# Kernel optimization log

Hardware: AMD Instinct MI355X
Metric: run time of the kernel (lower is better)

Reference implementation:

```python
import jax, jax.numpy as jnp
import numpy as np

DIM = 768
HEADS = 12
FRAMES = 16
T = FRAMES // 2          # temporal length per stream = 8
N = 196                  # spatial patch tokens (14x14)
B = 16                   # batch
SCALE = (DIM // HEADS) ** -0.5


def setup_inputs() -> dict:
    key = jax.random.key(0)
    ks = jax.random.split(key, 10)
    return {
        "s_x": jax.random.normal(ks[0], (N + 1, B * T, DIM), jnp.float32),
        "t_x": jax.random.normal(ks[1], (B, T * N, DIM), jnp.float32),
        "clip_time_pos": SCALE * jax.random.normal(ks[2], (T, DIM), jnp.float32),
        "vmae_time_pos": SCALE * jax.random.normal(ks[3], (T, DIM), jnp.float32),
        "Wq": jax.random.normal(ks[4], (DIM, DIM), jnp.float32) * 0.02,
        "q_bias": jnp.zeros((DIM,), jnp.float32),
        "Wkv": jax.random.normal(ks[5], (2 * DIM, DIM), jnp.float32) * 0.02,
        "kv_bias": jnp.zeros((2 * DIM,), jnp.float32),
        "Wproj": jax.random.normal(ks[6], (DIM, DIM), jnp.float32) * 0.02,
        "proj_bias": jnp.zeros((DIM,), jnp.float32),
    }


def reference(s_x, t_x, clip_time_pos, vmae_time_pos,
              Wq, q_bias, Wkv, kv_bias, Wproj, proj_bias):
    b = t_x.shape[0]
    t = s_x.shape[1] // b            # = FRAMES // 2
    n = s_x.shape[0] - 1             # spatial tokens (CLS excluded)
    d = s_x.shape[-1]
    h = HEADS
    hd = d // h
    scale = hd ** -0.5

    s_cls = s_x[0]                                   # [b*t, d]
    # 'n (b t) d -> (b n) t d'
    s_pat = s_x[1:].reshape(n, b, t, d).transpose(1, 0, 2, 3).reshape(b * n, t, d)
    s_pat = s_pat + clip_time_pos                    # [(b n), t, d]
    # 'b (t n) d -> (b n) t d'
    tx = t_x.reshape(b, t, n, d).transpose(0, 2, 1, 3).reshape(b * n, t, d)
    tx = tx + vmae_time_pos

    # projections (bias added manually as in F.linear with explicit bias)
    q = (s_pat @ Wq.T + q_bias).reshape(b * n, t, h, hd).transpose(0, 2, 1, 3)  # [bn,h,t,hd]
    kv = (tx @ Wkv.T + kv_bias).reshape(b * n, t, 2, h, hd)                      # e outermost in (e h d)
    k = kv[:, :, 0].transpose(0, 2, 1, 3)            # [bn,h,t,hd]
    v = kv[:, :, 1].transpose(0, 2, 1, 3)

    attn = jax.nn.softmax(jnp.einsum('bhqd,bhkd->bhqk', q * scale, k), axis=-1)
    out = jnp.einsum('bhqk,bhkd->bhqd', attn, v)     # [bn,h,t,hd]
    out = out.transpose(0, 2, 1, 3).reshape(b * n, t, d)
    out = out @ Wproj.T + proj_bias
    # '(b n) t d -> n (b t) d'
    out = out.reshape(b, n, t, d).transpose(1, 0, 2, 3).reshape(n, b * t, d)
    return jnp.concatenate([s_cls[None], out], axis=0)
```

## Files before the change

### kernel.cpp

```cpp
#include <hip/hip_runtime.h>
#include <stdint.h>

#define DIM   768
#define NTOK  196
#define TT    8
#define MROWS 25088
#define HEADS 12
#define NKT   12

typedef __bf16 bf16x8 __attribute__((ext_vector_type(8)));
typedef float  f32x4  __attribute__((ext_vector_type(4)));
typedef unsigned short u16x4 __attribute__((ext_vector_type(4)));
typedef unsigned short u16x8 __attribute__((ext_vector_type(8)));

typedef __attribute__((address_space(1))) const void GAS;
typedef __attribute__((address_space(3))) void LAS;

__device__ inline unsigned short f2bf(float f) {
  uint32_t u = __builtin_bit_cast(uint32_t, f);
  u += 0x7FFFu + ((u >> 16) & 1u);
  return (unsigned short)(u >> 16);
}
__device__ inline float bf2f(unsigned short s) {
  uint32_t u = ((uint32_t)s) << 16;
  return __builtin_bit_cast(float, u);
}
__device__ inline void gl_lds16(const unsigned short* g, unsigned short* l) {
  __builtin_amdgcn_global_load_lds((GAS*)g, (LAS*)l, 16, 0, 0);
}
__device__ inline int xcd_swz(int orig, int nwg) {
  int xcd = orig & 7, loc = orig >> 3;
  int q = nwg >> 3, r = nwg & 7;
  int base = (xcd < r) ? xcd * (q + 1) : r * (q + 1) + (xcd - r) * q;
  return base + loc;
}

#define WAITV(n) asm volatile("s_waitcnt vmcnt(" #n ")" ::: "memory")

__global__ void wprep_kernel(const float* __restrict__ wq,
                             const float* __restrict__ wkv,
                             const float* __restrict__ wproj,
                             unsigned short* __restrict__ out) {
  int idx4 = blockIdx.x * blockDim.x + threadIdx.x;
  const int total4 = 2359296 / 4;
  if (idx4 >= total4) return;
  int e = idx4 * 4;
  const float* src; int off;
  if (e < 589824)        { src = wq;    off = e; }
  else if (e < 1769472)  { src = wkv;   off = e - 589824; }
  else                   { src = wproj; off = e - 1769472; }
  f32x4 v = *reinterpret_cast<const f32x4*>(&src[off]);
  u16x4 o;
  o[0] = f2bf(v[0]); o[1] = f2bf(v[1]); o[2] = f2bf(v[2]); o[3] = f2bf(v[3]);
  *reinterpret_cast<u16x4*>(&out[e]) = o;
}

__global__ void cls_kernel(const float* __restrict__ sx, float* __restrict__ out) {
  int i4 = blockIdx.x * blockDim.x + threadIdx.x;
  if (i4 < (128 * 768) / 4)
    reinterpret_cast<f32x4*>(out)[i4] = reinterpret_cast<const f32x4*>(sx)[i4];
}

template<int MODE>
__global__ __launch_bounds__(256)
void aprep_kernel(const float* __restrict__ src, const float* __restrict__ timepos,
                  unsigned short* __restrict__ dst) {
  int idx = blockIdx.x * blockDim.x + threadIdx.x;
  const int total = MROWS * (DIM / 8);
  if (idx >= total) return;
  int m  = idx / 96;
  int c8 = (idx - m * 96) * 8;
  int bn = m >> 3, t = m & 7;
  int b  = bn / NTOK, n = bn - b * NTOK;
  int srow = (MODE == 0) ? ((1 + n) * 128 + b * 8 + t)
                         : (b * (TT * NTOK) + t * NTOK + n);
  const float* sp = &src[srow * DIM + c8];
  const float* pp = &timepos[t * DIM + c8];
  f32x4 a0 = reinterpret_cast<const f32x4*>(sp)[0];
  f32x4 a1 = reinterpret_cast<const f32x4*>(sp)[1];
  f32x4 p0 = reinterpret_cast<const f32x4*>(pp)[0];
  f32x4 p1 = reinterpret_cast<const f32x4*>(pp)[1];
  a0 += p0; a1 += p1;
  u16x8 o;
  o[0] = f2bf(a0[0]); o[1] = f2bf(a0[1]); o[2] = f2bf(a0[2]); o[3] = f2bf(a0[3]);
  o[4] = f2bf(a1[0]); o[5] = f2bf(a1[1]); o[6] = f2bf(a1[2]); o[7] = f2bf(a1[3]);
  *reinterpret_cast<u16x8*>(&dst[m * DIM + c8]) = o;
}

template<int MODE>
__global__ __launch_bounds__(512)
void gemm8(const unsigned short* __restrict__ As,
           const unsigned short* __restrict__ At,
           const unsigned short* __restrict__ W0,
           const unsigned short* __restrict__ W1,
           const float* __restrict__ b0,
           const float* __restrict__ b1,
           unsigned short* __restrict__ out0,
           unsigned short* __restrict__ out1,
           float* __restrict__ fout,
           int bid0) {
  __shared__ unsigned short SB[3 * 24576];

  const int tid  = threadIdx.x;
  const int lane = tid & 63;
  const int w    = tid >> 6;
  const int wm   = w >> 2;
  const int wn   = w & 3;

  int bid = xcd_swz(blockIdx.x, gridDim.x) + bid0;

  const unsigned short *Ag, *Wg;
  const float* bias;
  unsigned short* ob = nullptr;
  int rt, ct, Ncols;
  float scale = 1.0f;
  if (MODE == 0) {
    if (bid < 588) { rt = bid / 6;  ct = bid % 6;  Ag = As; Wg = W0; bias = b0; ob = out0; Ncols = 768;  scale = 0.125f; }
    else { int b2 = bid - 588; rt = b2 / 12; ct = b2 % 12; Ag = At; Wg = W1; bias = b1; ob = out1; Ncols = 1536; }
  } else {
    rt = bid / 6; ct = bid % 6; Ag = As; Wg = W0; bias = b0; Ncols = 768;
  }
  const int m0 = rt * 256;
  const int n0 = ct * 128;

  auto stageA = [&](int kt) {
    const int kb = kt * 64;
    unsigned short* dst = &SB[(kt % 3) * 24576];
    #pragma unroll
    for (int rnd = 0; rnd < 4; ++rnd) {
      int s    = rnd * 8 + w;
      int srow = s * 8 + (lane >> 3);
      int scol = ((lane & 7) * 8) ^ ((srow & 7) << 3);
      gl_lds16(&Ag[(size_t)(m0 + srow) * 768 + kb + scol], dst + s * 512);
    }
  };
  auto stageB = [&](int kt) {
    const int kb = kt * 64;
    unsigned short* dst = &SB[(kt % 3) * 24576 + 16384];
    #pragma unroll
    for (int rnd = 0; rnd < 2; ++rnd) {
      int s    = rnd * 8 + w;
      int srow = s * 8 + (lane >> 3);
      int scol = ((lane & 7) * 8) ^ ((srow & 7) << 3);
      gl_lds16(&Wg[(size_t)(n0 + srow) * 768 + kb + scol], dst + s * 512);
    }
  };

  f32x4 acc[8][2] = {};

  stageA(0); stageB(0);
  stageA(1); stageB(1);

  for (int kt = 0; kt < NKT; ++kt) {
    __builtin_amdgcn_sched_barrier(0);
    if (kt < NKT - 1) { WAITV(6); } else { WAITV(0); }
    __builtin_amdgcn_s_barrier();
    asm volatile("" ::: "memory");

    const unsigned short* Ab = &SB[(kt % 3) * 24576];
    const unsigned short* Bb = Ab + 16384;
    const bool st = (kt + 2) < NKT;

    if (st) stageA(kt + 2);
    __builtin_amdgcn_sched_barrier(0);

    #pragma unroll
    for (int ks = 0; ks < 2; ++ks) {
      bf16x8 af[8], bfv[2];
      const int kc = ks * 32 + (lane >> 4) * 8;
      #pragma unroll
      for (int fm = 0; fm < 8; ++fm) {
        int r = wm * 128 + fm * 16 + (lane & 15);
        af[fm] = *reinterpret_cast<const bf16x8*>(&Ab[r * 64 + (kc ^ ((r & 7) << 3))]);
      }
      #pragma unroll
      for (int fn = 0; fn < 2; ++fn) {
        int r = wn * 32 + fn * 16 + (lane & 15);
        bfv[fn] = *reinterpret_cast<const bf16x8*>(&Bb[r * 64 + (kc ^ ((r & 7) << 3))]);
      }
      __builtin_amdgcn_s_setprio(1);
      #pragma unroll
      for (int fm = 0; fm < 8; ++fm)
        #pragma unroll
        for (int fn = 0; fn < 2; ++fn)
          acc[fm][fn] = __builtin_amdgcn_mfma_f32_16x16x32_bf16(af[fm], bfv[fn], acc[fm][fn], 0, 0, 0);
      __builtin_amdgcn_s_setprio(0);
      if (ks == 0 && st) stageB(kt + 2);
      __builtin_amdgcn_sched_barrier(0);
    }
  }

  #pragma unroll
  for (int fm = 0; fm < 8; ++fm) {
    #pragma unroll
    for (int fn = 0; fn < 2; ++fn) {
      int col = n0 + wn * 32 + fn * 16 + (lane & 15);
      float bsv = bias[col];
      #pragma unroll
      for (int i = 0; i < 4; ++i) {
        int row = m0 + wm * 128 + fm * 16 + (lane >> 4) * 4 + i;
        float v = acc[fm][fn][i] + bsv;
        if (MODE == 0) {
          v *= scale;
          ob[(size_t)row * Ncols + col] = f2bf(v);
        } else {
          int bn = row >> 3, t = row & 7;
          int b  = bn / NTOK, n = bn - b * NTOK;
          fout[((1 + n) * 128 + b * 8 + t) * DIM + col] = v;
        }
      }
    }
  }
}

__global__ __launch_bounds__(256)
void attn_kernel(const unsigned short* __restrict__ qb,
                 const unsigned short* __restrict__ kvb,
                 unsigned short* __restrict__ ob) {
  __shared__ __align__(16) float lds[4][3][8][68];
  const int tid  = threadIdx.x;
  const int lane = tid & 63;
  const int w    = tid >> 6;
  const int wid  = blockIdx.x * 4 + w;
  const int bn   = wid / HEADS;
  const int h    = wid - bn * HEADS;

  const int t  = lane >> 3;
  const int d0 = (lane & 7) * 8;
  const int qoff = (bn * 8 + t) * DIM + h * 64 + d0;
  const int koff = (bn * 8 + t) * (2 * DIM) + h * 64 + d0;

  u16x8 q8 = *reinterpret_cast<const u16x8*>(&qb[qoff]);
  u16x8 k8 = *reinterpret_cast<const u16x8*>(&kvb[koff]);
  u16x8 v8 = *reinterpret_cast<const u16x8*>(&kvb[koff + DIM]);
  f32x4 qa, qc, ka, kc, va, vc;
  #pragma unroll
  for (int e = 0; e < 4; ++e) {
    qa[e] = bf2f(q8[e]); qc[e] = bf2f(q8[e + 4]);
    ka[e] = bf2f(k8[e]); kc[e] = bf2f(k8[e + 4]);
    va[e] = bf2f(v8[e]); vc[e] = bf2f(v8[e + 4]);
  }
  *reinterpret_cast<f32x4*>(&lds[w][0][t][d0])     = qa;
  *reinterpret_cast<f32x4*>(&lds[w][0][t][d0 + 4]) = qc;
  *reinterpret_cast<f32x4*>(&lds[w][1][t][d0])     = ka;
  *reinterpret_cast<f32x4*>(&lds[w][1][t][d0 + 4]) = kc;
  *reinterpret_cast<f32x4*>(&lds[w][2][t][d0])     = va;
  *reinterpret_cast<f32x4*>(&lds[w][2][t][d0 + 4]) = vc;
  __syncthreads();

  const int i = lane >> 3, j = lane & 7;
  const f32x4* qi = reinterpret_cast<const f32x4*>(&lds[w][0][i][0]);
  const f32x4* kj = reinterpret_cast<const f32x4*>(&lds[w][1][j][0]);
  float s = 0.f;
  #pragma unroll
  for (int c = 0; c < 16; ++c) {
    f32x4 a = qi[c], b = kj[c];
    s += a[0] * b[0] + a[1] * b[1] + a[2] * b[2] + a[3] * b[3];
  }
  float m = s;
  m = fmaxf(m, __shfl_xor(m, 1));
  m = fmaxf(m, __shfl_xor(m, 2));
  m = fmaxf(m, __shfl_xor(m, 4));
  float e = __expf(s - m);
  float sum = e;
  sum += __shfl_xor(sum, 1);
  sum += __shfl_xor(sum, 2);
  sum += __shfl_xor(sum, 4);
  float p = e / sum;

  float o[8] = {};
  #pragma unroll
  for (int jj = 0; jj < 8; ++jj) {
    float pj = __shfl(p, (lane & 56) | jj);
    const f32x4* vj = reinterpret_cast<const f32x4*>(&lds[w][2][jj][d0]);
    f32x4 v0 = vj[0], v1 = vj[1];
    o[0] += pj * v0[0]; o[1] += pj * v0[1]; o[2] += pj * v0[2]; o[3] += pj * v0[3];
    o[4] += pj * v1[0]; o[5] += pj * v1[1]; o[6] += pj * v1[2]; o[7] += pj * v1[3];
  }
  u16x8 os;
  #pragma unroll
  for (int e2 = 0; e2 < 8; ++e2) os[e2] = f2bf(o[e2]);
  *reinterpret_cast<u16x8*>(&ob[qoff]) = os;
}

extern "C" void kernel_launch(void* const* d_in, const int* in_sizes, int n_in,
                              void* d_out, int out_size, void* d_ws, size_t ws_size,
                              hipStream_t stream) {
  const float* s_x       = (const float*)d_in[0];
  const float* t_x       = (const float*)d_in[1];
  const float* clip_pos  = (const float*)d_in[2];
  const float* vmae_pos  = (const float*)d_in[3];
  const float* Wq        = (const float*)d_in[4];
  const float* q_bias    = (const float*)d_in[5];
  const float* Wkv       = (const float*)d_in[6];
  const float* kv_bias   = (const float*)d_in[7];
  const float* Wproj     = (const float*)d_in[8];
  const float* proj_bias = (const float*)d_in[9];
  float* out = (float*)d_out;

  char* ws = (char*)d_ws;
  unsigned short* w_bf = (unsigned short*)ws;
  const size_t ABUF = 38535168, KVB = 77070336, WB = 4718592;
  const bool merged = ws_size >= (WB + 3 * ABUF + KVB);

  const unsigned short* wq_bf = w_bf;
  const unsigned short* wkv_bf = w_bf + 589824;
  const unsigned short* wpj_bf = w_bf + 1769472;

  const int prep_blocks = (MROWS * 96 + 255) / 256;

  wprep_kernel<<<dim3((589824 + 255) / 256), dim3(256), 0, stream>>>(Wq, Wkv, Wproj, w_bf);
  cls_kernel<<<dim3(96), dim3(256), 0, stream>>>(s_x, out);

  if (merged) {
    unsigned short* As    = (unsigned short*)(ws + WB);
    unsigned short* At    = (unsigned short*)(ws + WB + ABUF);
    unsigned short* q_bf  = (unsigned short*)(ws + WB + 2 * ABUF);
    unsigned short* kv_bf = (unsigned short*)(ws + WB + 3 * ABUF);
    aprep_kernel<0><<<dim3(prep_blocks), dim3(256), 0, stream>>>(s_x, clip_pos, As);
    aprep_kernel<1><<<dim3(prep_blocks), dim3(256), 0, stream>>>(t_x, vmae_pos, At);
    gemm8<0><<<dim3(1764), dim3(512), 0, stream>>>(As, At, wq_bf, wkv_bf, q_bias, kv_bias,
                                                   q_bf, kv_bf, nullptr, 0);
    attn_kernel<<<dim3(9408), dim3(256), 0, stream>>>(q_bf, kv_bf, As);
    gemm8<1><<<dim3(588), dim3(512), 0, stream>>>(As, nullptr, wpj_bf, nullptr, proj_bias,
                                                  nullptr, nullptr, nullptr, out, 0);
  } else {
    unsigned short* buf1  = (unsigned short*)(ws + WB);
    unsigned short* q_bf  = (unsigned short*)(ws + WB + ABUF);
    unsigned short* kv_bf = (unsigned short*)(ws + WB + 2 * ABUF);
    aprep_kernel<0><<<dim3(prep_blocks), dim3(256), 0, stream>>>(s_x, clip_pos, buf1);
    gemm8<0><<<dim3(588), dim3(512), 0, stream>>>(buf1, buf1, wq_bf, wkv_bf, q_bias, kv_bias,
                                                  q_bf, kv_bf, nullptr, 0);
    aprep_kernel<1><<<dim3(prep_blocks), dim3(256), 0, stream>>>(t_x, vmae_pos, buf1);
    gemm8<0><<<dim3(1176), dim3(512), 0, stream>>>(buf1, buf1, wq_bf, wkv_bf, q_bias, kv_bias,
                                                   q_bf, kv_bf, nullptr, 588);
    attn_kernel<<<dim3(9408), dim3(256), 0, stream>>>(q_bf, kv_bf, buf1);
    gemm8<1><<<dim3(588), dim3(512), 0, stream>>>(buf1, nullptr, wpj_bf, nullptr, proj_bias,
                                                  nullptr, nullptr, nullptr, out, 0);
  }
}
```

Measured before the change: 212.4 us.

## Use 256x256 ping-pong tiled GEMM with quadrant phases for Q/KV projections

Measured after the change: 220.7 us. 3.9% more time.

```diff
diff --git a/kernel.cpp b/kernel.cpp
--- a/kernel.cpp
+++ b/kernel.cpp
@@ -36,6 +36,8 @@
 }
 
 #define WAITV(n) asm volatile("s_waitcnt vmcnt(" #n ")" ::: "memory")
+#define CFENCE   asm volatile("" ::: "memory")
+#define TBAR     do { CFENCE; __builtin_amdgcn_s_barrier(); CFENCE; } while (0)
 
 __global__ void wprep_kernel(const float* __restrict__ wq,
                              const float* __restrict__ wkv,
@@ -87,20 +89,58 @@
   *reinterpret_cast<u16x8*>(&dst[m * DIM + c8]) = o;
 }
 
-template<int MODE>
-__global__ __launch_bounds__(512)
-void gemm8(const unsigned short* __restrict__ As,
-           const unsigned short* __restrict__ At,
-           const unsigned short* __restrict__ W0,
-           const unsigned short* __restrict__ W1,
-           const float* __restrict__ b0,
-           const float* __restrict__ b1,
-           unsigned short* __restrict__ out0,
-           unsigned short* __restrict__ out1,
-           float* __restrict__ fout,
-           int bid0) {
-  __shared__ unsigned short SB[3 * 24576];
-
+#define PHASE(buf, mq, nq, RA, STG)                                           \
+  {                                                                           \
+    const unsigned short* As_ = &SB[((buf) * 4 + (mq)) * 8192];               \
+    const unsigned short* Bs_ = &SB[((buf) * 4 + 2 + (nq)) * 8192];           \
+    if (RA) {                                                                 \
+      _Pragma("unroll")                                                       \
+      for (int ks = 0; ks < 2; ++ks)                                          \
+        _Pragma("unroll")                                                     \
+        for (int fm = 0; fm < 4; ++fm) {                                      \
+          int r = wm * 64 + fm * 16 + (lane & 15);                            \
+          int c = ks * 32 + (lane >> 4) * 8;                                  \
+          af[ks][fm] = *reinterpret_cast<const bf16x8*>(                      \
+              &As_[r * 64 + (c ^ ((r & 7) << 3))]);                           \
+        }                                                                     \
+    }                                                                         \
+    bf16x8 bfv[2][2];                                                         \
+    _Pragma("unroll")                                                         \
+    for (int ks = 0; ks < 2; ++ks)                                            \
+      _Pragma("unroll")                                                       \
+      for (int fn = 0; fn < 2; ++fn) {                                        \
+        int r = wn * 32 + fn * 16 + (lane & 15);                              \
+        int c = ks * 32 + (lane >> 4) * 8;                                    \
+        bfv[ks][fn] = *reinterpret_cast<const bf16x8*>(                       \
+            &Bs_[r * 64 + (c ^ ((r & 7) << 3))]);                             \
+      }                                                                       \
+    STG;                                                                      \
+    TBAR;                                                                     \
+    asm volatile("s_waitcnt lgkmcnt(0)" ::: "memory");                        \
+    __builtin_amdgcn_sched_barrier(0);                                        \
+    __builtin_amdgcn_s_setprio(1);                                            \
+    _Pragma("unroll")                                                         \
+    for (int ks = 0; ks < 2; ++ks)                                            \
+      _Pragma("unroll")                                                       \
+      for (int fm = 0; fm < 4; ++fm)                                          \
+        _Pragma("unroll")                                                     \
+        for (int fn = 0; fn < 2; ++fn)                                        \
+          acc[mq][nq][fm][fn] = __builtin_amdgcn_mfma_f32_16x16x32_bf16(      \
+              af[ks][fm], bfv[ks][fn], acc[mq][nq][fm][fn], 0, 0, 0);         \
+    __builtin_amdgcn_s_setprio(0);                                            \
+  }
+
+__global__ __launch_bounds__(512, 1)
+void gemm8p(const unsigned short* __restrict__ As,
+            const unsigned short* __restrict__ At,
+            const unsigned short* __restrict__ Wqb,
+            const unsigned short* __restrict__ Wkvb,
+            const float* __restrict__ bq,
+            const float* __restrict__ bkv,
+            unsigned short* __restrict__ qo,
+            unsigned short* __restrict__ kvo,
+            int bid0) {
+  __shared__ unsigned short SB[8 * 8192];
   const int tid  = threadIdx.x;
   const int lane = tid & 63;
   const int w    = tid >> 6;
@@ -108,20 +148,100 @@
   const int wn   = w & 3;
 
   int bid = xcd_swz(blockIdx.x, gridDim.x) + bid0;
-
-  const unsigned short *Ag, *Wg;
-  const float* bias;
-  unsigned short* ob = nullptr;
-  int rt, ct, Ncols;
-  float scale = 1.0f;
-  if (MODE == 0) {
-    if (bid < 588) { rt = bid / 6;  ct = bid % 6;  Ag = As; Wg = W0; bias = b0; ob = out0; Ncols = 768;  scale = 0.125f; }
-    else { int b2 = bid - 588; rt = b2 / 12; ct = b2 % 12; Ag = At; Wg = W1; bias = b1; ob = out1; Ncols = 1536; }
-  } else {
-    rt = bid / 6; ct = bid % 6; Ag = As; Wg = W0; bias = b0; Ncols = 768;
-  }
-  const int m0 = rt * 256;
-  const int n0 = ct * 128;
+  const unsigned short *Ag, *Wg; const float* bias;
+  unsigned short* ob; int rt, ct, Ncols; bool isq;
+  if (bid < 294) { isq = true;  rt = bid / 3; ct = bid % 3; Ag = As; Wg = Wqb;  bias = bq;  ob = qo;  Ncols = 768; }
+  else { isq = false; int b2 = bid - 294; rt = b2 / 6; ct = b2 % 6; Ag = At; Wg = Wkvb; bias = bkv; ob = kvo; Ncols = 1536; }
+  const int m0 = rt * 256, n0 = ct * 256;
+
+  float bsv[2][2];
+  #pragma unroll
+  for (int q = 0; q < 2; ++q)
+    #pragma unroll
+    for (int fn = 0; fn < 2; ++fn)
+      bsv[q][fn] = bias[n0 + q * 128 + wn * 32 + fn * 16 + (lane & 15)];
+
+  auto stage = [&](int slot, const unsigned short* src, int base_row, int kt) {
+    unsigned short* dst = &SB[slot * 8192];
+    #pragma unroll
+    for (int rr = 0; rr < 2; ++rr) {
+      int srow = rr * 64 + w * 8 + (lane >> 3);
+      int scol = ((lane & 7) * 8) ^ ((srow & 7) << 3);
+      gl_lds16(&src[(size_t)(base_row + srow) * DIM + kt * 64 + scol],
+               dst + (rr * 512 + w * 64) * 8);
+    }
+  };
+
+  f32x4 acc[2][2][4][2] = {};
+
+  stage(0, Ag, m0,       0);
+  stage(1, Ag, m0 + 128, 0);
+  stage(2, Wg, n0,       0);
+  stage(3, Wg, n0 + 128, 0);
+  stage(4, Ag, m0,       1);
+  stage(6, Wg, n0,       1);
+  WAITV(4);
+  TBAR;
+
+  for (int i = 0; i < NKT / 2; ++i) {
+    const int kt1 = 2 * i + 1, kt2 = 2 * i + 2, kt3 = 2 * i + 3;
+    const bool g2 = kt2 < NKT, g3 = kt3 < NKT, last = (i == NKT / 2 - 1);
+    bf16x8 af[2][4];
+
+    PHASE(0, 0, 0, 1, (stage(5, Ag, m0 + 128, kt1)));
+    TBAR;
+    PHASE(0, 0, 1, 0, (stage(7, Wg, n0 + 128, kt1)));
+    TBAR;
+    PHASE(0, 1, 0, 1, (g2 ? stage(0, Ag, m0, kt2) : void()));
+    TBAR;
+    PHASE(0, 1, 1, 0, (g2 ? stage(2, Wg, n0, kt2) : void()));
+    if (last) { WAITV(0); } else { WAITV(4); }
+    TBAR;
+    PHASE(1, 0, 0, 1, (g2 ? stage(1, Ag, m0 + 128, kt2) : void()));
+    TBAR;
+    PHASE(1, 0, 1, 0, (g2 ? stage(3, Wg, n0 + 128, kt2) : void()));
+    TBAR;
+    PHASE(1, 1, 0, 1, (g3 ? stage(4, Ag, m0, kt3) : void()));
+    TBAR;
+    PHASE(1, 1, 1, 0, (g3 ? stage(6, Wg, n0, kt3) : void()));
+    if (!last) { WAITV(4); }
+    TBAR;
+  }
+
+  #pragma unroll
+  for (int mq = 0; mq < 2; ++mq)
+    #pragma unroll
+    for (int nq = 0; nq < 2; ++nq)
+      #pragma unroll
+      for (int fm = 0; fm < 4; ++fm)
+        #pragma unroll
+        for (int fn = 0; fn < 2; ++fn) {
+          int col = n0 + nq * 128 + wn * 32 + fn * 16 + (lane & 15);
+          #pragma unroll
+          for (int ii = 0; ii < 4; ++ii) {
+            int row = m0 + mq * 128 + wm * 64 + fm * 16 + (lane >> 4) * 4 + ii;
+            float v = acc[mq][nq][fm][fn][ii] + bsv[nq][fn];
+            if (isq) v *= 0.125f;
+            ob[(size_t)row * Ncols + col] = f2bf(v);
+          }
+        }
+}
+
+__global__ __launch_bounds__(512)
+void gemm_proj(const unsigned short* __restrict__ Ag,
+               const unsigned short* __restrict__ Wg,
+               const float* __restrict__ bias,
+               float* __restrict__ fout) {
+  __shared__ unsigned short SB[3 * 24576];
+
+  const int tid  = threadIdx.x;
+  const int lane = tid & 63;
+  const int w    = tid >> 6;
+  const int wm   = w >> 2, wn = w & 3;
+
+  int bid = xcd_swz(blockIdx.x, gridDim.x);
+  const int rt = bid / 6, ct = bid % 6;
+  const int m0 = rt * 256, n0 = ct * 128;
 
   auto stageA = [&](int kt) {
     const int kb = kt * 64;
@@ -155,7 +275,7 @@
     __builtin_amdgcn_sched_barrier(0);
     if (kt < NKT - 1) { WAITV(6); } else { WAITV(0); }
     __builtin_amdgcn_s_barrier();
-    asm volatile("" ::: "memory");
+    CFENCE;
 
     const unsigned short* Ab = &SB[(kt % 3) * 24576];
     const unsigned short* Bb = Ab + 16384;
@@ -200,14 +320,9 @@
       for (int i = 0; i < 4; ++i) {
         int row = m0 + wm * 128 + fm * 16 + (lane >> 4) * 4 + i;
         float v = acc[fm][fn][i] + bsv;
-        if (MODE == 0) {
-          v *= scale;
-          ob[(size_t)row * Ncols + col] = f2bf(v);
-        } else {
-          int bn = row >> 3, t = row & 7;
-          int b  = bn / NTOK, n = bn - b * NTOK;
-          fout[((1 + n) * 128 + b * 8 + t) * DIM + col] = v;
-        }
+        int bn = row >> 3, t = row & 7;
+        int b  = bn / NTOK, n = bn - b * NTOK;
+        fout[((1 + n) * 128 + b * 8 + t) * DIM + col] = v;
       }
     }
   }
@@ -303,7 +418,7 @@
   const size_t ABUF = 38535168, KVB = 77070336, WB = 4718592;
   const bool merged = ws_size >= (WB + 3 * ABUF + KVB);
 
-  const unsigned short* wq_bf = w_bf;
+  const unsigned short* wq_bf  = w_bf;
   const unsigned short* wkv_bf = w_bf + 589824;
   const unsigned short* wpj_bf = w_bf + 1769472;
 
@@ -319,23 +434,21 @@
     unsigned short* kv_bf = (unsigned short*)(ws + WB + 3 * ABUF);
     aprep_kernel<0><<<dim3(prep_blocks), dim3(256), 0, stream>>>(s_x, clip_pos, As);
     aprep_kernel<1><<<dim3(prep_blocks), dim3(256), 0, stream>>>(t_x, vmae_pos, At);
-    gemm8<0><<<dim3(1764), dim3(512), 0, stream>>>(As, At, wq_bf, wkv_bf, q_bias, kv_bias,
-                                                   q_bf, kv_bf, nullptr, 0);
+    gemm8p<<<dim3(882), dim3(512), 0, stream>>>(As, At, wq_bf, wkv_bf, q_bias, kv_bias,
+                                                q_bf, kv_bf, 0);
     attn_kernel<<<dim3(9408), dim3(256), 0, stream>>>(q_bf, kv_bf, As);
-    gemm8<1><<<dim3(588), dim3(512), 0, stream>>>(As, nullptr, wpj_bf, nullptr, proj_bias,
-                                                  nullptr, nullptr, nullptr, out, 0);
+    gemm_proj<<<dim3(588), dim3(512), 0, stream>>>(As, wpj_bf, proj_bias, out);
   } else {
     unsigned short* buf1  = (unsigned short*)(ws + WB);
     unsigned short* q_bf  = (unsigned short*)(ws + WB + ABUF);
     unsigned short* kv_bf = (unsigned short*)(ws + WB + 2 * ABUF);
     aprep_kernel<0><<<dim3(prep_blocks), dim3(256), 0, stream>>>(s_x, clip_pos, buf1);
-    gemm8<0><<<dim3(588), dim3(512), 0, stream>>>(buf1, buf1, wq_bf, wkv_bf, q_bias, kv_bias,
-                                                  q_bf, kv_bf, nullptr, 0);
+    gemm8p<<<dim3(294), dim3(512), 0, stream>>>(buf1, buf1, wq_bf, wkv_bf, q_bias, kv_bias,
+                                                q_bf, kv_bf, 0);
     aprep_kernel<1><<<dim3(prep_blocks), dim3(256), 0, stream>>>(t_x, vmae_pos, buf1);
-    gemm8<0><<<dim3(1176), dim3(512), 0, stream>>>(buf1, buf1, wq_bf, wkv_bf, q_bias, kv_bias,
-                                                   q_bf, kv_bf, nullptr, 588);
+    gemm8p<<<dim3(588), dim3(512), 0, stream>>>(buf1, buf1, wq_bf, wkv_bf, q_bias, kv_bias,
+                                                q_bf, kv_bf, 294);
     attn_kernel<<<dim3(9408), dim3(256), 0, stream>>>(q_bf, kv_bf, buf1);
-    gemm8<1><<<dim3(588), dim3(512), 0, stream>>>(buf1, nullptr, wpj_bf, nullptr, proj_bias,
-                                                  nullptr, nullptr, nullptr, out, 0);
-  }
-}
+    gemm_proj<<<dim3(588), dim3(512), 0, stream>>>(buf1, wpj_bf, proj_bias, out);
+  }
+}
```
